# Kernel tuning notes

Measured on AMD Instinct MI355X. Metric: run time of the kernel, lower is better.

## Reference

```python
import jax, jax.numpy as jnp
import numpy as np

B = 512
N_DRUGS = 4096
H_DRUG = 1023          # per-drug feature dim; input to MLP is 2*(H_DRUG+1) = 2048
N_CELL = 32
DIMS = [2048, 2048, 1024, 512, 1]


def setup_inputs() -> dict:
    key = jax.random.key(0)
    ks = jax.random.split(key, 12)
    pairs = jax.random.randint(ks[0], (B, 2), 0, N_DRUGS)
    cell_lines = jax.random.randint(ks[1], (B,), 0, N_CELL)
    attrs = jax.random.normal(ks[2], (B, 4), dtype=jnp.float32)
    h_drug = jax.random.normal(ks[3], (N_DRUGS, H_DRUG), dtype=jnp.float32)
    # shared Linear layers (torch Linear: y = x @ W.T + b), kaiming-uniform-ish init
    def lin(k, fan_in, fan_out):
        k1, k2 = jax.random.split(k)
        bound = 1.0 / np.sqrt(fan_in)
        W = jax.random.uniform(k1, (fan_out, fan_in), jnp.float32, -bound, bound)
        b = jax.random.uniform(k2, (fan_out,), jnp.float32, -bound, bound)
        return W, b
    W0, b0 = lin(ks[4], DIMS[0], DIMS[1])
    W1, b1 = lin(ks[5], DIMS[1], DIMS[2])
    # cell-line specific layers: 1/100 * randn
    L0 = 0.01 * jax.random.normal(ks[6], (N_CELL, DIMS[3], DIMS[2]), dtype=jnp.float32)
    O0 = 0.01 * jax.random.normal(ks[7], (N_CELL, DIMS[3], 1), dtype=jnp.float32)
    L1 = 0.01 * jax.random.normal(ks[8], (N_CELL, DIMS[4], DIMS[3]), dtype=jnp.float32)
    O1 = 0.01 * jax.random.normal(ks[9], (N_CELL, DIMS[4], 1), dtype=jnp.float32)
    return {"pairs": pairs, "cell_lines": cell_lines, "attrs": attrs, "h_drug": h_drug,
            "W0": W0, "b0": b0, "W1": W1, "b1": b1,
            "L0": L0, "O0": O0, "L1": L1, "O1": O1}


def reference(pairs, cell_lines, attrs, h_drug, W0, b0, W1, b1, L0, O0, L1, O1):
    n_attr = attrs.shape[1] // 2
    h1 = h_drug[pairs[:, 0]]                               # [B, H_DRUG]
    h2 = h_drug[pairs[:, 1]]
    bd1 = jnp.concatenate([h1, attrs[:, n_attr - 1:n_attr]], axis=1)
    bd2 = jnp.concatenate([h2, attrs[:, -1:]], axis=1)
    # original flips order with p=0.5 (data augmentation); fixed to (bd1, bd2) for determinism
    x = jnp.concatenate([bd1, bd2], axis=1)                # [B, 2048]
    # shared MLP (note: original applies relu(relu(x)) == relu(x))
    x = jax.nn.relu(x @ W0.T + b0)                         # [B, 2048]
    x = jax.nn.relu(x @ W1.T + b1)                         # [B, 1024]
    # cell-line-specific layers: gather per-sample weight and batched matvec
    x = jax.nn.relu(jnp.einsum('boi,bi->bo', L0[cell_lines], x) + O0[cell_lines, :, 0])  # [B, 512]
    x = jnp.einsum('boi,bi->bo', L1[cell_lines], x) + O1[cell_lines, :, 0]               # [B, 1]
    return x[:, 0]
```

## Files before the change

kernel.cpp:

```cpp
#include <hip/hip_runtime.h>

typedef short s16x8 __attribute__((ext_vector_type(8)));
typedef float f32x4 __attribute__((ext_vector_type(4)));
typedef unsigned short u16;

#define BATCH 512
#define HD    1023
#define K0    2048
#define N0    2048
#define N1    1024
#define N2    512

__device__ __forceinline__ u16 f2bf(float f) {
  unsigned u = __builtin_bit_cast(unsigned, f);
  unsigned r = (u + 0x7fffu + ((u >> 16) & 1u)) >> 16;
  return (u16)r;
}

__device__ __forceinline__ s16x8 pack8(f32x4 a, f32x4 b) {
  union { unsigned u[4]; s16x8 v; } r;
  asm("v_cvt_pk_bf16_f32 %0, %1, %2" : "=v"(r.u[0]) : "v"(a[0]), "v"(a[1]));
  asm("v_cvt_pk_bf16_f32 %0, %1, %2" : "=v"(r.u[1]) : "v"(a[2]), "v"(a[3]));
  asm("v_cvt_pk_bf16_f32 %0, %1, %2" : "=v"(r.u[2]) : "v"(b[0]), "v"(b[1]));
  asm("v_cvt_pk_bf16_f32 %0, %1, %2" : "=v"(r.u[3]) : "v"(b[2]), "v"(b[3]));
  return r.v;
}

__global__ __launch_bounds__(256) void k_prep(
    const int* __restrict__ pairs, const float* __restrict__ attrs,
    const float* __restrict__ h_drug, const float* __restrict__ W0,
    const int* __restrict__ cells, const float* __restrict__ O1,
    u16* __restrict__ xb, u16* __restrict__ w0b, float* __restrict__ out) {
  const int bid = blockIdx.x, tid = threadIdx.x;
  if (bid < 512) {
    const int b = bid;
    const float* h0 = h_drug + (size_t)pairs[2 * b] * HD;
    const float* h1 = h_drug + (size_t)pairs[2 * b + 1] * HD;
    u16* xr = xb + (size_t)b * K0;
    for (int i = tid; i < HD; i += 256) {
      xr[i] = f2bf(h0[i]);
      xr[1024 + i] = f2bf(h1[i]);
    }
    if (tid == 0) {
      xr[1023] = f2bf(attrs[4 * b + 1]);
      xr[2047] = f2bf(attrs[4 * b + 3]);
      out[b] = O1[cells[b]];
    }
  } else {
    const size_t e = ((size_t)(bid - 512) * 256 + tid) * 16;
    f32x4 a = *(const f32x4*)(W0 + e),     b2 = *(const f32x4*)(W0 + e + 4);
    f32x4 c = *(const f32x4*)(W0 + e + 8), d  = *(const f32x4*)(W0 + e + 12);
    *(s16x8*)(w0b + e)     = pack8(a, b2);
    *(s16x8*)(w0b + e + 8) = pack8(c, d);
  }
}

#define GI1(s, t) { \
  pa_##s = *(const s16x8*)(agp0 + (size_t)(t) * 128); \
  pb_##s = *(const s16x8*)(bgp0 + (size_t)(t) * 128); }

#define GS1(s, t, DOLOAD) { \
  char* buf = lds[(s) & 1]; \
  *(s16x8*)(buf + awo0) = pa_##s; \
  *(s16x8*)(buf + 8192 + awo0) = pb_##s; \
  asm volatile("s_waitcnt lgkmcnt(0)" ::: "memory"); \
  __builtin_amdgcn_s_barrier(); \
  asm volatile("" ::: "memory"); \
  if (DOLOAD) GI1(s, (t) + 4) \
  __builtin_amdgcn_s_setprio(1); \
  _Pragma("unroll") \
  for (int ks = 0; ks < 2; ++ks) { \
    const int kq = ((ks << 6) | lk) ^ sw; \
    s16x8 a0 = *(const s16x8*)(buf + aoff + kq); \
    s16x8 a1 = *(const s16x8*)(buf + aoff + 2048 + kq); \
    s16x8 b0 = *(const s16x8*)(buf + 8192 + boff + kq); \
    acc0 = __builtin_amdgcn_mfma_f32_16x16x32_bf16(a0, b0, acc0, 0, 0, 0); \
    acc1 = __builtin_amdgcn_mfma_f32_16x16x32_bf16(a1, b0, acc1, 0, 0, 0); \
  } \
  __builtin_amdgcn_s_setprio(0); }

__global__ __launch_bounds__(512) void k_gemm1(
    const u16* __restrict__ A, const u16* __restrict__ B,
    const float* __restrict__ bias, u16* __restrict__ Y,
    const float* __restrict__ W1f, u16* __restrict__ w1b) {
  constexpr int K = 2048, N = 2048;
  if (blockIdx.x >= 256) {
    const size_t e = (((size_t)blockIdx.x - 256) * 512 + threadIdx.x) * 8;
    f32x4 a = *(const f32x4*)(W1f + e), b2 = *(const f32x4*)(W1f + e + 4);
    *(s16x8*)(w1b + e) = pack8(a, b2);
    return;
  }
  __shared__ char lds[2][16384];
  const int tid = threadIdx.x;
  const int w = tid >> 6, l = tid & 63;
  const int wr = w >> 2, wn = w & 3;
  const int lrow = l & 15;
  const int lk = (l >> 4) << 4;
  const int sw = (lrow & 7) << 4;

  const int wgid = (blockIdx.x & 7) * 32 + (blockIdx.x >> 3);
  const int bn = wgid >> 3, bm = wgid & 7;

  const size_t K2 = (size_t)K * 2;
  const char* Ag = (const char*)A + (size_t)bm * 64 * K2;
  const char* Bg = (const char*)B + (size_t)bn * 64 * K2;

  const int o0 = tid * 16;
  const int ar0 = o0 >> 7, ac0 = o0 & 127;
  const char* agp0 = Ag + (size_t)ar0 * K2 + ac0;
  const char* bgp0 = Bg + (size_t)ar0 * K2 + ac0;
  const int awo0 = (ar0 << 7) + (ac0 ^ ((ar0 & 7) << 4));

  const int aoff = (wr * 32 + lrow) * 128;
  const int boff = (wn * 16 + lrow) * 128;

  f32x4 acc0 = {}, acc1 = {};
  s16x8 pa_0, pa_1, pa_2, pa_3;
  s16x8 pb_0, pb_1, pb_2, pb_3;

  GI1(0, 0) GI1(1, 1) GI1(2, 2) GI1(3, 3)
  constexpr int NT = 32;
  int t = 0;
  for (; t < NT - 4; t += 4) {
    GS1(0, t, 1) GS1(1, t + 1, 1) GS1(2, t + 2, 1) GS1(3, t + 3, 1)
  }
  GS1(0, t, 0) GS1(1, t + 1, 0) GS1(2, t + 2, 0) GS1(3, t + 3, 0)

  const int colg = bn * 64 + wn * 16 + lrow;
  const int rowb = bm * 64 + wr * 32 + ((l >> 4) << 2);
  const float bv = bias[colg];
#pragma unroll
  for (int fa = 0; fa < 2; ++fa)
#pragma unroll
    for (int r = 0; r < 4; ++r) {
      float v = (fa ? acc1 : acc0)[r] + bv;
      v = v > 0.f ? v : 0.f;
      Y[(size_t)(rowb + fa * 16 + r) * N + colg] = f2bf(v);
    }
}

#define GI(s, t) { \
  pa0_##s = *(const s16x8*)(agp0 + (size_t)(t) * 128); \
  pb_##s = *(const s16x8*)(bgp0 + (size_t)(t) * 128); }

#define GS(s, t, DOLOAD) { \
  char* buf = lds[(s) & 1]; \
  *(s16x8*)(buf + awo0) = pa0_##s; \
  *(s16x8*)(buf + ABYTES + awo0) = pb_##s; \
  asm volatile("s_waitcnt lgkmcnt(0)" ::: "memory"); \
  __builtin_amdgcn_s_barrier(); \
  asm volatile("" ::: "memory"); \
  if (DOLOAD) GI(s, (t) + 4) \
  __builtin_amdgcn_s_setprio(1); \
  _Pragma("unroll") \
  for (int ks = 0; ks < 2; ++ks) { \
    const int kq = ((ks << 6) | lk) ^ sw; \
    s16x8 a0 = *(const s16x8*)(buf + aoff + kq); \
    s16x8 b0 = *(const s16x8*)(buf + ABYTES + boff + kq); \
    acc0 = __builtin_amdgcn_mfma_f32_16x16x32_bf16(a0, b0, acc0, 0, 0, 0); \
  } \
  __builtin_amdgcn_s_setprio(0); }

__global__ __launch_bounds__(256) void k_gemm2(
    const u16* __restrict__ A, const u16* __restrict__ B,
    const float* __restrict__ bias, u16* __restrict__ Y) {
  constexpr int K = 2048, N = 1024;
  constexpr int ABYTES = 32 * 128;
  __shared__ char lds[2][ABYTES + 4096];
  const int tid = threadIdx.x;
  const int w = tid >> 6, l = tid & 63;
  const int wr = w >> 1, wc = w & 1;
  const int lrow = l & 15;
  const int lk = (l >> 4) << 4;
  const int sw = (lrow & 7) << 4;

  const int wgid = (blockIdx.x & 7) * 64 + (blockIdx.x >> 3);
  const int bn = wgid >> 4, bm = wgid & 15;

  const size_t K2 = (size_t)K * 2;
  const char* Ag = (const char*)A + (size_t)bm * 32 * K2;
  const char* Bg = (const char*)B + (size_t)(bn * 32) * K2;

  const int o0 = tid * 16;
  const int ar0 = o0 >> 7, ac0 = o0 & 127;
  const char* agp0 = Ag + (size_t)ar0 * K2 + ac0;
  const char* bgp0 = Bg + (size_t)ar0 * K2 + ac0;
  const int awo0 = (ar0 << 7) + (ac0 ^ ((ar0 & 7) << 4));

  const int aoff = (wr * 16 + lrow) * 128;
  const int boff = (wc * 16 + lrow) * 128;

  f32x4 acc0 = {};
  s16x8 pa0_0, pa0_1, pa0_2, pa0_3;
  s16x8 pb_0, pb_1, pb_2, pb_3;

  GI(0, 0) GI(1, 1) GI(2, 2) GI(3, 3)
  constexpr int NT = 32;
  int t = 0;
  for (; t < NT - 4; t += 4) {
    GS(0, t, 1) GS(1, t + 1, 1) GS(2, t + 2, 1) GS(3, t + 3, 1)
  }
  GS(0, t, 0) GS(1, t + 1, 0) GS(2, t + 2, 0) GS(3, t + 3, 0)

  const int colg = bn * 32 + wc * 16 + lrow;
  const int rowb = bm * 32 + wr * 16 + ((l >> 4) << 2);
  const float bv = bias[colg];
#pragma unroll
  for (int r = 0; r < 4; ++r) {
    float v = acc0[r] + bv;
    v = v > 0.f ? v : 0.f;
    Y[(size_t)(rowb + r) * N + colg] = f2bf(v);
  }
}

#define H_ISSUE(S, ch) { \
  const float* src = hsrc + (ch) * 256; \
  q0_##S = *(const f32x4*)(src);      q1_##S = *(const f32x4*)(src + 4); \
  q2_##S = *(const f32x4*)(src + 8);  q3_##S = *(const f32x4*)(src + 12); \
  q4_##S = *(const f32x4*)(src + 16); q5_##S = *(const f32x4*)(src + 20); \
  q6_##S = *(const f32x4*)(src + 24); q7_##S = *(const f32x4*)(src + 28); }

#define H_WRITE(S, ch) { \
  char* dst = lbuf[(ch) & 1] + (hrow << 9); \
  *(s16x8*)(dst + ((hcb + 0)  ^ hswz)) = pack8(q0_##S, q1_##S); \
  *(s16x8*)(dst + ((hcb + 16) ^ hswz)) = pack8(q2_##S, q3_##S); \
  *(s16x8*)(dst + ((hcb + 32) ^ hswz)) = pack8(q4_##S, q5_##S); \
  *(s16x8*)(dst + ((hcb + 48) ^ hswz)) = pack8(q6_##S, q7_##S); }

#define H_SYNC { \
  asm volatile("s_waitcnt lgkmcnt(0)" ::: "memory"); \
  __builtin_amdgcn_s_barrier(); \
  asm volatile("" ::: "memory"); }

#define H_MFMA(ch) { \
  const char* bb = lbuf[(ch) & 1]; \
  s16x8 bv0 = *(const s16x8*)(bb + ((0 * 16 + lrow) << 9) + kboff); \
  s16x8 bv1 = *(const s16x8*)(bb + ((1 * 16 + lrow) << 9) + kboff); \
  s16x8 bv2 = *(const s16x8*)(bb + ((2 * 16 + lrow) << 9) + kboff); \
  s16x8 bv3 = *(const s16x8*)(bb + ((3 * 16 + lrow) << 9) + kboff); \
  s16x8 av0 = *(const s16x8*)(ap0 + (ch) * 256); \
  s16x8 av1 = *(const s16x8*)(ap1 + (ch) * 256); \
  __builtin_amdgcn_s_setprio(1); \
  acc[0][0] = __builtin_amdgcn_mfma_f32_16x16x32_bf16(av0, bv0, acc[0][0], 0, 0, 0); \
  acc[0][1] = __builtin_amdgcn_mfma_f32_16x16x32_bf16(av0, bv1, acc[0][1], 0, 0, 0); \
  acc[0][2] = __builtin_amdgcn_mfma_f32_16x16x32_bf16(av0, bv2, acc[0][2], 0, 0, 0); \
  acc[0][3] = __builtin_amdgcn_mfma_f32_16x16x32_bf16(av0, bv3, acc[0][3], 0, 0, 0); \
  acc[1][0] = __builtin_amdgcn_mfma_f32_16x16x32_bf16(av1, bv0, acc[1][0], 0, 0, 0); \
  acc[1][1] = __builtin_amdgcn_mfma_f32_16x16x32_bf16(av1, bv1, acc[1][1], 0, 0, 0); \
  acc[1][2] = __builtin_amdgcn_mfma_f32_16x16x32_bf16(av1, bv2, acc[1][2], 0, 0, 0); \
  acc[1][3] = __builtin_amdgcn_mfma_f32_16x16x32_bf16(av1, bv3, acc[1][3], 0, 0, 0); \
  __builtin_amdgcn_s_setprio(0); }

__global__ __launch_bounds__(512) void k_head(
    const int* __restrict__ cells, const u16* __restrict__ y2b,
    const float* __restrict__ L0, const float* __restrict__ O0,
    const float* __restrict__ L1, float* __restrict__ out) {
  __shared__ int slist[544];
  __shared__ int scnt;
  __shared__ float red[8][2048];
  __shared__ char lbuf[2][32768];
  const int tid = threadIdx.x;
  const int c = blockIdx.x >> 3, rt = blockIdx.x & 7;
  if (tid == 0) scnt = 0;
  __syncthreads();
  for (int i = tid; i < BATCH; i += 512)
    if (cells[i] == c) slist[atomicAdd(&scnt, 1)] = i;
  __syncthreads();
  const int ns = scnt;
  if (ns == 0) return;
  const int npad = (ns + 31) & ~31;
  for (int i = ns + tid; i < npad; i += 512) slist[i] = slist[0];
  __syncthreads();

  const int w = tid >> 6, l = tid & 63;
  const int lrow = l & 15;
  const int r0 = rt * 64;
  const float* L0c = L0 + ((size_t)c * N2 + r0) * N1;
  const int hrow = tid >> 3;
  const int hcb = (tid & 7) * 64;
  const int hswz = (hrow & 7) << 4;
  const float* hsrc = L0c + (size_t)hrow * N1 + (tid & 7) * 32;
  const int kboff = ((w * 64 + ((l >> 4) << 4)) ^ ((lrow & 7) << 4));

  f32x4 q0_A, q1_A, q2_A, q3_A, q4_A, q5_A, q6_A, q7_A;
  f32x4 q0_B, q1_B, q2_B, q3_B, q4_B, q5_B, q6_B, q7_B;

  for (int cb = 0; cb < npad; cb += 32) {
    const u16* ap0 = y2b + (size_t)slist[cb + lrow] * N1 + w * 32 + ((l >> 4) << 3);
    const u16* ap1 = y2b + (size_t)slist[cb + 16 + lrow] * N1 + w * 32 + ((l >> 4) << 3);
    f32x4 acc[2][4] = {};
    H_ISSUE(A, 0)
    H_WRITE(A, 0)
    H_ISSUE(B, 1)
    H_SYNC
    H_MFMA(0)
    H_WRITE(B, 1)
    H_ISSUE(A, 2)
    H_SYNC
    H_MFMA(1)
    H_WRITE(A, 2)
    H_ISSUE(B, 3)
    H_SYNC
    H_MFMA(2)
    H_WRITE(B, 3)
    H_SYNC
    H_MFMA(3)

    __syncthreads();
#pragma unroll
    for (int h = 0; h < 2; ++h)
#pragma unroll
      for (int fb = 0; fb < 4; ++fb)
#pragma unroll
        for (int r = 0; r < 4; ++r) {
          const int s0 = h * 16 + (l >> 4) * 4 + r;
          red[w][s0 * 64 + fb * 16 + lrow] = acc[h][fb][r];
        }
    __syncthreads();
    {
      const int s = tid >> 4;
      const int rq = (tid & 15) * 4;
      if (cb + s < ns) {
        float p = 0.f;
#pragma unroll
        for (int j = 0; j < 4; ++j) {
          const int r = rq + j, e = s * 64 + r;
          float v = red[0][e] + red[1][e] + red[2][e] + red[3][e] +
                    red[4][e] + red[5][e] + red[6][e] + red[7][e] +
                    O0[(size_t)c * N2 + r0 + r];
          v = v > 0.f ? v : 0.f;
          p += v * L1[(size_t)c * N2 + r0 + r];
        }
#pragma unroll
        for (int off = 8; off; off >>= 1) p += __shfl_xor(p, off, 16);
        if ((tid & 15) == 0) atomicAdd(&out[slist[cb + s]], p);
      }
    }
  }
}

extern "C" void kernel_launch(void* const* d_in, const int* in_sizes, int n_in,
                              void* d_out, int out_size, void* d_ws, size_t ws_size,
                              hipStream_t stream) {
  const int*   pairs  = (const int*)d_in[0];
  const int*   cells  = (const int*)d_in[1];
  const float* attrs  = (const float*)d_in[2];
  const float* h_drug = (const float*)d_in[3];
  const float* W0     = (const float*)d_in[4];
  const float* b0     = (const float*)d_in[5];
  const float* W1     = (const float*)d_in[6];
  const float* b1     = (const float*)d_in[7];
  const float* L0     = (const float*)d_in[8];
  const float* O0     = (const float*)d_in[9];
  const float* L1     = (const float*)d_in[10];
  const float* O1     = (const float*)d_in[11];
  float* out = (float*)d_out;

  char* ws = (char*)d_ws;
  u16* xb  = (u16*)(ws);
  u16* w0b = (u16*)(ws + (2u  << 20));
  u16* w1b = (u16*)(ws + (10u << 20));
  u16* y1b = (u16*)(ws + (14u << 20));
  u16* y2b = (u16*)(ws + (16u << 20));

  k_prep<<<1536, 256, 0, stream>>>(pairs, attrs, h_drug, W0, cells, O1,
                                   xb, w0b, out);
  k_gemm1<<<768, 512, 0, stream>>>(xb, w0b, b0, y1b, W1, w1b);
  k_gemm2<<<512, 256, 0, stream>>>(y1b, w1b, b1, y2b);
  k_head<<<256, 512, 0, stream>>>(cells, y2b, L0, O0, L1, out);
}
```

Baseline: 46.22 us.

## Double K-tile depth in both GEMMs, widen gemm2 tile, vectorize gather

Both GEMM kernels now stage a 128-wide K slice per step instead of 64, halving the number of barrier-synchronized iterations, with a 16-row XOR swizzle for the wider LDS rows. gemm2 moves to 512-thread blocks computing 32x64 tiles over 256 blocks instead of 32x32 tiles over 512 blocks, improving B reuse. The prep gather now converts 8 floats per thread with vector loads and packed stores, and the attribute column is folded into the last chunk. Costs are more LDS per block and more prefetch registers, which may lower occupancy, and fewer gemm2 blocks for the GPU's many CUs.

```diff
diff --git a/kernel.cpp b/kernel.cpp
--- a/kernel.cpp
+++ b/kernel.cpp
@@ -24,6 +24,10 @@
   asm("v_cvt_pk_bf16_f32 %0, %1, %2" : "=v"(r.u[2]) : "v"(b[0]), "v"(b[1]));
   asm("v_cvt_pk_bf16_f32 %0, %1, %2" : "=v"(r.u[3]) : "v"(b[2]), "v"(b[3]));
   return r.v;
+}
+
+__device__ __forceinline__ f32x4 ld4u(const float* p) {
+  f32x4 v; __builtin_memcpy(&v, p, 16); return v;
 }
 
 __global__ __launch_bounds__(256) void k_prep(
@@ -34,18 +38,20 @@
   const int bid = blockIdx.x, tid = threadIdx.x;
   if (bid < 512) {
     const int b = bid;
-    const float* h0 = h_drug + (size_t)pairs[2 * b] * HD;
-    const float* h1 = h_drug + (size_t)pairs[2 * b + 1] * HD;
-    u16* xr = xb + (size_t)b * K0;
-    for (int i = tid; i < HD; i += 256) {
-      xr[i] = f2bf(h0[i]);
-      xr[1024 + i] = f2bf(h1[i]);
+    const int half = tid >> 7, ch = tid & 127;
+    const float* h = h_drug + (size_t)pairs[2 * b + half] * HD;
+    u16* xr = xb + (size_t)b * K0 + half * 1024;
+    f32x4 v0, v1;
+    if (ch < 127) {
+      v0 = ld4u(h + ch * 8);
+      v1 = ld4u(h + ch * 8 + 4);
+    } else {
+      v0 = ld4u(h + 1016);
+      v1[0] = h[1020]; v1[1] = h[1021]; v1[2] = h[1022];
+      v1[3] = attrs[4 * b + 1 + 2 * half];
     }
-    if (tid == 0) {
-      xr[1023] = f2bf(attrs[4 * b + 1]);
-      xr[2047] = f2bf(attrs[4 * b + 3]);
-      out[b] = O1[cells[b]];
-    }
+    *(s16x8*)(xr + ch * 8) = pack8(v0, v1);
+    if (tid == 0) out[b] = O1[cells[b]];
   } else {
     const size_t e = ((size_t)(bid - 512) * 256 + tid) * 16;
     f32x4 a = *(const f32x4*)(W0 + e),     b2 = *(const f32x4*)(W0 + e + 4);
@@ -56,24 +62,28 @@
 }
 
 #define GI1(s, t) { \
-  pa_##s = *(const s16x8*)(agp0 + (size_t)(t) * 128); \
-  pb_##s = *(const s16x8*)(bgp0 + (size_t)(t) * 128); }
+  pa0_##s = *(const s16x8*)(agp0 + (size_t)(t) * 256); \
+  pa1_##s = *(const s16x8*)(agp1 + (size_t)(t) * 256); \
+  pb0_##s = *(const s16x8*)(bgp0 + (size_t)(t) * 256); \
+  pb1_##s = *(const s16x8*)(bgp1 + (size_t)(t) * 256); }
 
 #define GS1(s, t, DOLOAD) { \
   char* buf = lds[(s) & 1]; \
-  *(s16x8*)(buf + awo0) = pa_##s; \
-  *(s16x8*)(buf + 8192 + awo0) = pb_##s; \
+  *(s16x8*)(buf + awo0) = pa0_##s; \
+  *(s16x8*)(buf + awo1) = pa1_##s; \
+  *(s16x8*)(buf + 16384 + awo0) = pb0_##s; \
+  *(s16x8*)(buf + 16384 + awo1) = pb1_##s; \
   asm volatile("s_waitcnt lgkmcnt(0)" ::: "memory"); \
   __builtin_amdgcn_s_barrier(); \
   asm volatile("" ::: "memory"); \
   if (DOLOAD) GI1(s, (t) + 4) \
   __builtin_amdgcn_s_setprio(1); \
   _Pragma("unroll") \
-  for (int ks = 0; ks < 2; ++ks) { \
-    const int kq = ((ks << 6) | lk) ^ sw; \
+  for (int ks = 0; ks < 4; ++ks) { \
+    const int kq = ((ks << 6) | lk) ^ swz; \
     s16x8 a0 = *(const s16x8*)(buf + aoff + kq); \
-    s16x8 a1 = *(const s16x8*)(buf + aoff + 2048 + kq); \
-    s16x8 b0 = *(const s16x8*)(buf + 8192 + boff + kq); \
+    s16x8 a1 = *(const s16x8*)(buf + aoff + 4096 + kq); \
+    s16x8 b0 = *(const s16x8*)(buf + 16384 + boff + kq); \
     acc0 = __builtin_amdgcn_mfma_f32_16x16x32_bf16(a0, b0, acc0, 0, 0, 0); \
     acc1 = __builtin_amdgcn_mfma_f32_16x16x32_bf16(a1, b0, acc1, 0, 0, 0); \
   } \
@@ -90,13 +100,13 @@
     *(s16x8*)(w1b + e) = pack8(a, b2);
     return;
   }
-  __shared__ char lds[2][16384];
+  __shared__ char lds[2][32768];
   const int tid = threadIdx.x;
   const int w = tid >> 6, l = tid & 63;
   const int wr = w >> 2, wn = w & 3;
   const int lrow = l & 15;
   const int lk = (l >> 4) << 4;
-  const int sw = (lrow & 7) << 4;
+  const int swz = lrow << 4;
 
   const int wgid = (blockIdx.x & 7) * 32 + (blockIdx.x >> 3);
   const int bn = wgid >> 3, bm = wgid & 7;
@@ -106,20 +116,27 @@
   const char* Bg = (const char*)B + (size_t)bn * 64 * K2;
 
   const int o0 = tid * 16;
-  const int ar0 = o0 >> 7, ac0 = o0 & 127;
+  const int ar0 = o0 >> 8, ac0 = o0 & 255;
   const char* agp0 = Ag + (size_t)ar0 * K2 + ac0;
   const char* bgp0 = Bg + (size_t)ar0 * K2 + ac0;
-  const int awo0 = (ar0 << 7) + (ac0 ^ ((ar0 & 7) << 4));
-
-  const int aoff = (wr * 32 + lrow) * 128;
-  const int boff = (wn * 16 + lrow) * 128;
+  const int awo0 = (ar0 << 8) + (ac0 ^ ((ar0 & 15) << 4));
+  const int o1 = o0 + 8192;
+  const int ar1 = o1 >> 8, ac1 = o1 & 255;
+  const char* agp1 = Ag + (size_t)ar1 * K2 + ac1;
+  const char* bgp1 = Bg + (size_t)ar1 * K2 + ac1;
+  const int awo1 = (ar1 << 8) + (ac1 ^ ((ar1 & 15) << 4));
+
+  const int aoff = (wr * 32 + lrow) * 256;
+  const int boff = (wn * 16 + lrow) * 256;
 
   f32x4 acc0 = {}, acc1 = {};
-  s16x8 pa_0, pa_1, pa_2, pa_3;
-  s16x8 pb_0, pb_1, pb_2, pb_3;
+  s16x8 pa0_0, pa0_1, pa0_2, pa0_3;
+  s16x8 pa1_0, pa1_1, pa1_2, pa1_3;
+  s16x8 pb0_0, pb0_1, pb0_2, pb0_3;
+  s16x8 pb1_0, pb1_1, pb1_2, pb1_3;
 
   GI1(0, 0) GI1(1, 1) GI1(2, 2) GI1(3, 3)
-  constexpr int NT = 32;
+  constexpr int NT = 16;
   int t = 0;
   for (; t < NT - 4; t += 4) {
     GS1(0, t, 1) GS1(1, t + 1, 1) GS1(2, t + 2, 1) GS1(3, t + 3, 1)
@@ -139,70 +156,77 @@
     }
 }
 
-#define GI(s, t) { \
-  pa0_##s = *(const s16x8*)(agp0 + (size_t)(t) * 128); \
-  pb_##s = *(const s16x8*)(bgp0 + (size_t)(t) * 128); }
-
-#define GS(s, t, DOLOAD) { \
+#define GI2(s, t) { \
+  pa_##s = *(const s16x8*)(agp0 + (size_t)(t) * 256); \
+  pb0_##s = *(const s16x8*)(bgp0 + (size_t)(t) * 256); \
+  pb1_##s = *(const s16x8*)(bgp1 + (size_t)(t) * 256); }
+
+#define GS2(s, t, DOLOAD) { \
   char* buf = lds[(s) & 1]; \
-  *(s16x8*)(buf + awo0) = pa0_##s; \
-  *(s16x8*)(buf + ABYTES + awo0) = pb_##s; \
+  *(s16x8*)(buf + awo0) = pa_##s; \
+  *(s16x8*)(buf + 8192 + bwo0) = pb0_##s; \
+  *(s16x8*)(buf + 8192 + bwo1) = pb1_##s; \
   asm volatile("s_waitcnt lgkmcnt(0)" ::: "memory"); \
   __builtin_amdgcn_s_barrier(); \
   asm volatile("" ::: "memory"); \
-  if (DOLOAD) GI(s, (t) + 4) \
+  if (DOLOAD) GI2(s, (t) + 4) \
   __builtin_amdgcn_s_setprio(1); \
   _Pragma("unroll") \
-  for (int ks = 0; ks < 2; ++ks) { \
-    const int kq = ((ks << 6) | lk) ^ sw; \
+  for (int ks = 0; ks < 4; ++ks) { \
+    const int kq = ((ks << 6) | lk) ^ swz; \
     s16x8 a0 = *(const s16x8*)(buf + aoff + kq); \
-    s16x8 b0 = *(const s16x8*)(buf + ABYTES + boff + kq); \
+    s16x8 b0 = *(const s16x8*)(buf + 8192 + boff + kq); \
     acc0 = __builtin_amdgcn_mfma_f32_16x16x32_bf16(a0, b0, acc0, 0, 0, 0); \
   } \
   __builtin_amdgcn_s_setprio(0); }
 
-__global__ __launch_bounds__(256) void k_gemm2(
+__global__ __launch_bounds__(512) void k_gemm2(
     const u16* __restrict__ A, const u16* __restrict__ B,
     const float* __restrict__ bias, u16* __restrict__ Y) {
   constexpr int K = 2048, N = 1024;
-  constexpr int ABYTES = 32 * 128;
-  __shared__ char lds[2][ABYTES + 4096];
+  __shared__ char lds[2][24576];
   const int tid = threadIdx.x;
   const int w = tid >> 6, l = tid & 63;
-  const int wr = w >> 1, wc = w & 1;
+  const int wr = w >> 2, wn = w & 3;
   const int lrow = l & 15;
   const int lk = (l >> 4) << 4;
-  const int sw = (lrow & 7) << 4;
-
-  const int wgid = (blockIdx.x & 7) * 64 + (blockIdx.x >> 3);
+  const int swz = lrow << 4;
+
+  const int wgid = (blockIdx.x & 7) * 32 + (blockIdx.x >> 3);
   const int bn = wgid >> 4, bm = wgid & 15;
 
   const size_t K2 = (size_t)K * 2;
   const char* Ag = (const char*)A + (size_t)bm * 32 * K2;
-  const char* Bg = (const char*)B + (size_t)(bn * 32) * K2;
+  const char* Bg = (const char*)B + (size_t)bn * 64 * K2;
 
   const int o0 = tid * 16;
-  const int ar0 = o0 >> 7, ac0 = o0 & 127;
+  const int ar0 = o0 >> 8, ac0 = o0 & 255;
   const char* agp0 = Ag + (size_t)ar0 * K2 + ac0;
+  const int awo0 = (ar0 << 8) + (ac0 ^ ((ar0 & 15) << 4));
   const char* bgp0 = Bg + (size_t)ar0 * K2 + ac0;
-  const int awo0 = (ar0 << 7) + (ac0 ^ ((ar0 & 7) << 4));
-
-  const int aoff = (wr * 16 + lrow) * 128;
-  const int boff = (wc * 16 + lrow) * 128;
+  const int bwo0 = awo0;
+  const int o1 = o0 + 8192;
+  const int br1 = o1 >> 8, bc1 = o1 & 255;
+  const char* bgp1 = Bg + (size_t)br1 * K2 + bc1;
+  const int bwo1 = (br1 << 8) + (bc1 ^ ((br1 & 15) << 4));
+
+  const int aoff = (wr * 16 + lrow) * 256;
+  const int boff = (wn * 16 + lrow) * 256;
 
   f32x4 acc0 = {};
-  s16x8 pa0_0, pa0_1, pa0_2, pa0_3;
-  s16x8 pb_0, pb_1, pb_2, pb_3;
-
-  GI(0, 0) GI(1, 1) GI(2, 2) GI(3, 3)
-  constexpr int NT = 32;
+  s16x8 pa_0, pa_1, pa_2, pa_3;
+  s16x8 pb0_0, pb0_1, pb0_2, pb0_3;
+  s16x8 pb1_0, pb1_1, pb1_2, pb1_3;
+
+  GI2(0, 0) GI2(1, 1) GI2(2, 2) GI2(3, 3)
+  constexpr int NT = 16;
   int t = 0;
   for (; t < NT - 4; t += 4) {
-    GS(0, t, 1) GS(1, t + 1, 1) GS(2, t + 2, 1) GS(3, t + 3, 1)
-  }
-  GS(0, t, 0) GS(1, t + 1, 0) GS(2, t + 2, 0) GS(3, t + 3, 0)
-
-  const int colg = bn * 32 + wc * 16 + lrow;
+    GS2(0, t, 1) GS2(1, t + 1, 1) GS2(2, t + 2, 1) GS2(3, t + 3, 1)
+  }
+  GS2(0, t, 0) GS2(1, t + 1, 0) GS2(2, t + 2, 0) GS2(3, t + 3, 0)
+
+  const int colg = bn * 64 + wn * 16 + lrow;
   const int rowb = bm * 32 + wr * 16 + ((l >> 4) << 2);
   const float bv = bias[colg];
 #pragma unroll
@@ -366,6 +390,6 @@
   k_prep<<<1536, 256, 0, stream>>>(pairs, attrs, h_drug, W0, cells, O1,
                                    xb, w0b, out);
   k_gemm1<<<768, 512, 0, stream>>>(xb, w0b, b0, y1b, W1, w1b);
-  k_gemm2<<<512, 256, 0, stream>>>(y1b, w1b, b1, y2b);
+  k_gemm2<<<256, 512, 0, stream>>>(y1b, w1b, b1, y2b);
   k_head<<<256, 512, 0, stream>>>(cells, y2b, L0, O0, L1, out);
 }
```

New measurement: 45.03 us, median of 2. -2.6%, faster.
